# Performance work log

Hardware: AMD Instinct MI355X
Metric: run time of the kernel (lower is better)

Reference implementation:

```python
import jax, jax.numpy as jnp
import numpy as np


def setup_inputs() -> dict:
    key = jax.random.key(0)
    k1, k2 = jax.random.split(key)
    B, L, D = 8, 2048, 256
    x = jax.random.normal(k1, (B, L, D), dtype=jnp.float32)
    x_mask = jax.random.randint(k2, (B, L), 0, 2).astype(bool)  # True = padded key position
    return {"x": x, "x_mask": x_mask}


def reference(x, x_mask):
    # x: [B, L, D], x_mask: [B, L] bool (True = masked/padding)
    B, L, D = x.shape
    # Unscaled self-attention scores: [B, L, L]
    scores = jnp.einsum('bld,bmd->blm', x, x)
    # Diagonal exclusion: score of token with itself set to 0 (not -inf!)
    eye = jnp.eye(L, dtype=bool)
    scores = jnp.where(eye[None, :, :], jnp.float32(0.0), scores)
    # Padding mask: mask key columns with -inf (applied after diagonal zeroing,
    # so a masked diagonal entry ends up -inf, matching the torch order of ops)
    scores = jnp.where(x_mask[:, None, :], -jnp.inf, scores)
    a = jax.nn.softmax(scores, axis=2)
    return jnp.einsum('blm,bmd->bld', a, x)
```

## Files before the change

kernel.cpp:

```cpp
#include <hip/hip_runtime.h>
#include <hip/hip_bf16.h>

#define B_ 8
#define L_ 2048
#define D_ 256
#define BK 32
#define KSPLIT 2
#define KQ (L_/KSPLIT)
#define NIT (KQ/BK)
#define PSTR 40
#define NROW (B_*L_)
#define NE ((size_t)B_*L_*D_)
#define THR 6.0f
#define MINIT (-1e30f)

typedef __attribute__((ext_vector_type(8))) _Float16 f16x8;
typedef __attribute__((ext_vector_type(4))) _Float16 hf4;
typedef __attribute__((ext_vector_type(4))) float f32x4;

#define MFMA16F(a,b,c) __builtin_amdgcn_mfma_f32_16x16x32_f16((a),(b),(c),0,0,0)
#define NEG_INF (-__builtin_inff())
#define GLL(src,dst) __builtin_amdgcn_global_load_lds( \
    (const __attribute__((address_space(1))) void*)(src), \
    (__attribute__((address_space(3))) void*)(dst), 16, 0, 0)

__device__ __forceinline__ f32x4 fmax4(f32x4 a, f32x4 b){
  f32x4 r;
  r[0]=fmaxf(a[0],b[0]); r[1]=fmaxf(a[1],b[1]);
  r[2]=fmaxf(a[2],b[2]); r[3]=fmaxf(a[3],b[3]);
  return r;
}

__global__ void prep_k(const float* __restrict__ x,
                       _Float16* __restrict__ x16,
                       _Float16* __restrict__ vtl){
  __shared__ _Float16 T[64][258];
  const int t = threadIdx.x;
  const int l0 = blockIdx.x*64, b = blockIdx.y;
  const int r = t>>5, c = (t&31)*8;
  #pragma unroll
  for (int p=0;p<8;++p){
    int row = r + p*8;
    size_t idx = ((size_t)(b*L_ + l0 + row))*D_ + c;
    float4 v0 = *(const float4*)(x + idx);
    float4 v1 = *(const float4*)(x + idx + 4);
    f16x8 h;
    h[0]=(_Float16)v0.x; h[1]=(_Float16)v0.y; h[2]=(_Float16)v0.z; h[3]=(_Float16)v0.w;
    h[4]=(_Float16)v1.x; h[5]=(_Float16)v1.y; h[6]=(_Float16)v1.z; h[7]=(_Float16)v1.w;
    *(f16x8*)(x16 + idx) = h;
    #pragma unroll
    for (int j=0;j<8;++j) T[row][c+j] = h[j];
  }
  __syncthreads();
  _Float16* vb = vtl + ((size_t)(b*64 + blockIdx.x*2))*8192;
  #pragma unroll
  for (int i=0;i<8;++i){
    int n = t + 256*i;
    int q = n & 1023, tile = n>>10;
    int d = q>>2, ph = q&3;
    int kc = ph ^ ((d>>1)&3);
    int k0 = tile*32 + kc*8;
    f16x8 h;
    #pragma unroll
    for (int j=0;j<8;++j) h[j] = T[k0+j][d];
    *(f16x8*)(vb + (size_t)n*8) = h;
  }
}

__launch_bounds__(256, 2)
__global__ void flash_k(const _Float16* __restrict__ x16,
                        const _Float16* __restrict__ vtl,
                        const int* __restrict__ mask,
                        _Float16* __restrict__ oall,
                        float* __restrict__ mll,
                        float* __restrict__ mm){
  __shared__ __attribute__((aligned(16))) _Float16 sK[2][8192];
  __shared__ __attribute__((aligned(16))) _Float16 sV[2][8192];
  __shared__ __attribute__((aligned(16))) _Float16 sP[4][16*PSTR];

  const int tid  = threadIdx.x;
  const int wave = tid >> 6, lane = tid & 63;
  const int quad = lane >> 4, l16 = lane & 15;
  const int b = blockIdx.y, z = blockIdx.z;
  const int q0w = blockIdx.x*64 + wave*16;
  const int sw = l16 & 7, vsw = (l16>>1)&3;

  f16x8 qh[8];
  {
    const _Float16* qr = x16 + ((size_t)(b*L_ + q0w + l16))*D_;
    #pragma unroll
    for (int ks=0; ks<8; ++ks)
      qh[ks] = *(const f16x8*)(qr + ks*32 + quad*8);
  }
  unsigned long long mb = 0;
  {
    const int* mrow = mask + b*L_ + z*KQ;
    #pragma unroll
    for (int j=0;j<64;++j)
      mb |= (unsigned long long)(mrow[j*16 + l16] ? 1u : 0u) << j;
  }

  f32x4 M = (f32x4){MINIT, MINIT, MINIT, MINIT};

  unsigned kof[4], vof[4], dof[4];
  #pragma unroll
  for (int i=0;i<4;++i){
    int c = (wave + i*4)*64 + lane;
    int r = c>>5, pk = c&31;
    kof[i] = (unsigned)(r*512 + ((pk ^ (r&7))*16));
    vof[i] = (unsigned)(c*16);
    dof[i] = (unsigned)((wave + i*4)*1024);
  }
  const char* kbase = (const char*)x16 + ((size_t)b*L_ + (size_t)z*KQ)*(D_*2);
  const char* vbase = (const char*)vtl + ((size_t)(b*64 + z*32))*16384;

  #pragma unroll
  for (int i=0;i<4;++i){
    GLL(kbase + kof[i], (char*)sK[0] + dof[i]);
    GLL(vbase + vof[i], (char*)sV[0] + dof[i]);
  }

  f32x4 O[16], Osum;
  #pragma unroll
  for (int i=0;i<16;i++) O[i] = (f32x4){0.f,0.f,0.f,0.f};
  Osum = (f32x4){0.f,0.f,0.f,0.f};
  f16x8 ones;
  #pragma unroll
  for (int j=0;j<8;++j) ones[j] = (_Float16)1.0f;

  __syncthreads();

  for (int it=0; it<NIT; ++it){
    if (it+1 < NIT){
      const char* kb2 = kbase + (size_t)(it+1)*16384;
      const char* vb2 = vbase + (size_t)(it+1)*16384;
      char* kd = (char*)sK[(it+1)&1];
      char* vd = (char*)sV[(it+1)&1];
      #pragma unroll
      for (int i=0;i<4;++i){
        GLL(kb2 + kof[i], kd + dof[i]);
        GLL(vb2 + vof[i], vd + dof[i]);
      }
    }
    const _Float16* kb = sK[it&1];
    const _Float16* vb = sV[it&1];

    f32x4 S[2];
    S[0]=(f32x4){0,0,0,0}; S[1]=(f32x4){0,0,0,0};
    #pragma unroll
    for (int ks=0; ks<8; ++ks){
      f16x8 b0 = *(const f16x8*)(kb + (     l16)*256 + (((ks*4+quad)^sw)*8));
      f16x8 b1 = *(const f16x8*)(kb + (16 + l16)*256 + (((ks*4+quad)^sw)*8));
      S[0] = MFMA16F(qh[ks], b0, S[0]);
      S[1] = MFMA16F(qh[ks], b1, S[1]);
    }

    {
      const int d0 = q0w - (z*KQ + it*BK);
      if ((unsigned)d0 < 32u){
        const int ntd = d0 >> 4;
        #pragma unroll
        for (int r=0;r<4;++r)
          S[ntd][r] = (l16 == quad*4+r) ? 0.0f : S[ntd][r];
      }
    }
    {
      const unsigned mw = (unsigned)(mb >> (unsigned)(it*2));
      const float mk0 = (mw & 1u) ? NEG_INF : 0.0f;
      const float mk1 = (mw & 2u) ? NEG_INF : 0.0f;
      #pragma unroll
      for (int r=0;r<4;++r){ S[0][r] += mk0; S[1][r] += mk1; }
    }

    {
      int ok = 1;
      #pragma unroll
      for (int r=0;r<4;++r){
        ok &= (S[0][r] <= M[r] + THR);
        ok &= (S[1][r] <= M[r] + THR);
      }
      if (!__all(ok)){
        f32x4 t = fmax4(S[0], S[1]);
        #pragma unroll
        for (int off=1; off<16; off<<=1){
          f32x4 o;
          o[0]=__shfl_xor(t[0],off); o[1]=__shfl_xor(t[1],off);
          o[2]=__shfl_xor(t[2],off); o[3]=__shfl_xor(t[3],off);
          t = fmax4(t,o);
        }
        f32x4 mn = fmax4(M, t);
        float sc[4];
        #pragma unroll
        for (int r=0;r<4;++r) sc[r] = __expf(M[r] - mn[r]);
        #pragma unroll
        for (int vt=0; vt<16; ++vt){
          #pragma unroll
          for (int r=0;r<4;++r) O[vt][r] *= sc[r];
        }
        #pragma unroll
        for (int r=0;r<4;++r) Osum[r] *= sc[r];
        M = mn;
      }
    }

    #pragma unroll
    for (int r=0;r<4;++r){
      const int row = quad*4 + r;
      sP[wave][row*PSTR +      l16] = (_Float16)__expf(S[0][r] - M[r]);
      sP[wave][row*PSTR + 16 + l16] = (_Float16)__expf(S[1][r] - M[r]);
    }
    __threadfence_block();
    f16x8 pf = *(const f16x8*)(&sP[wave][l16*PSTR + quad*8]);

    #pragma unroll
    for (int vt=0; vt<16; ++vt){
      f16x8 bv = *(const f16x8*)(vb + (vt*16+l16)*32 + ((quad^vsw)*8));
      O[vt] = MFMA16F(pf, bv, O[vt]);
    }
    Osum = MFMA16F(pf, ones, Osum);

    __syncthreads();
  }

  {
    const int u = b*(L_/16) + blockIdx.x*4 + wave;
    _Float16* ob = oall + (size_t)z*NE + (size_t)u*4096;
    #pragma unroll
    for (int vt=0; vt<16; ++vt){
      hf4 hh;
      #pragma unroll
      for (int r=0;r<4;++r) hh[r] = (_Float16)O[vt][r];
      *(hf4*)(ob + vt*256 + lane*4) = hh;
    }
    if (l16 == 0){
      const int row = u*16 + quad*4;
      #pragma unroll
      for (int r=0;r<4;++r){
        mll[z*NROW + row + r] = Osum[r];
        mm [z*NROW + row + r] = M[r];
      }
    }
  }
}

__global__ void combine_k(float* __restrict__ out,
                          const _Float16* __restrict__ oall,
                          const float* __restrict__ mll,
                          const float* __restrict__ mm){
  __shared__ float T2[16][260];
  const int t = threadIdx.x, u = blockIdx.x;
  const int quad = (t>>4)&3, l16 = t&15;
  const int row0 = u*16 + quad*4;

  f32x4 mz[KSPLIT], lz[KSPLIT];
  #pragma unroll
  for (int zc=0; zc<KSPLIT; ++zc){
    mz[zc] = *(const f32x4*)(mm  + zc*NROW + row0);
    lz[zc] = *(const f32x4*)(mll + zc*NROW + row0);
  }
  f32x4 ms = mz[0];
  #pragma unroll
  for (int zc=1; zc<KSPLIT; ++zc) ms = fmax4(ms, mz[zc]);

  float sc[KSPLIT][4];
  f32x4 den = (f32x4){0.f,0.f,0.f,0.f};
  #pragma unroll
  for (int zc=0; zc<KSPLIT; ++zc){
    #pragma unroll
    for (int r=0;r<4;++r){
      sc[zc][r] = __expf(mz[zc][r] - ms[r]);
      den[r] += sc[zc][r] * lz[zc][r];
    }
  }
  float inv[4];
  #pragma unroll
  for (int r=0;r<4;++r) inv[r] = 1.0f/den[r];

  #pragma unroll
  for (int i=0;i<4;++i){
    const int f = t + 256*i;
    const int vt = f>>6;
    float acc[4] = {0.f,0.f,0.f,0.f};
    #pragma unroll
    for (int zc=0; zc<KSPLIT; ++zc){
      hf4 v = *(const hf4*)(oall + (size_t)zc*NE + (size_t)u*4096 + (size_t)f*4);
      #pragma unroll
      for (int r=0;r<4;++r) acc[r] += sc[zc][r] * (float)v[r];
    }
    #pragma unroll
    for (int r=0;r<4;++r) T2[quad*4+r][vt*16+l16] = acc[r]*inv[r];
  }
  __syncthreads();
  #pragma unroll
  for (int p=0;p<4;++p){
    const int row = (t>>6) + p*4, col = (t&63)*4;
    float4 vv = *(const float4*)&T2[row][col];
    *(float4*)(out + ((size_t)u*16 + row)*D_ + col) = vv;
  }
}

extern "C" void kernel_launch(void* const* d_in, const int* in_sizes, int n_in,
                              void* d_out, int out_size, void* d_ws, size_t ws_size,
                              hipStream_t stream) {
  const float* x    = (const float*)d_in[0];
  const int*   mask = (const int*)d_in[1];
  float*       out  = (float*)d_out;

  _Float16* x16  = (_Float16*)d_ws;
  _Float16* vtl  = x16 + NE;
  _Float16* oall = vtl + NE;
  float*    mll  = (float*)(oall + (size_t)KSPLIT*NE);
  float*    mm   = mll + (size_t)KSPLIT*NROW;

  prep_k   <<<dim3(L_/64, B_), dim3(256), 0, stream>>>(x, x16, vtl);
  flash_k  <<<dim3(L_/64, B_, KSPLIT), dim3(256), 0, stream>>>(x16, vtl, mask, oall, mll, mm);
  combine_k<<<dim3(NROW/16), dim3(256), 0, stream>>>(out, oall, mll, mm);
}
```

Measured before the change: 149.7 us.

## Process 32 query rows per wave to reuse K/V tiles across two query blocks

Each wave now handles two 16-row query blocks (128 queries per workgroup), so every K and V fragment loaded from LDS feeds two MFMAs instead of one. This halves the LDS traffic and global K/V loads per query and halves the grid. In exchange it doubles the O accumulators per wave, drops launch bounds to one block per CU, and leaves 256 workgroups, which lowers occupancy and latency hiding.

```diff
diff --git a/kernel.cpp b/kernel.cpp
--- a/kernel.cpp
+++ b/kernel.cpp
@@ -67,7 +67,7 @@
   }
 }
 
-__launch_bounds__(256, 2)
+__launch_bounds__(256, 1)
 __global__ void flash_k(const _Float16* __restrict__ x16,
                         const _Float16* __restrict__ vtl,
                         const int* __restrict__ mask,
@@ -76,21 +76,23 @@
                         float* __restrict__ mm){
   __shared__ __attribute__((aligned(16))) _Float16 sK[2][8192];
   __shared__ __attribute__((aligned(16))) _Float16 sV[2][8192];
-  __shared__ __attribute__((aligned(16))) _Float16 sP[4][16*PSTR];
+  __shared__ __attribute__((aligned(16))) _Float16 sP[4][32*PSTR];
 
   const int tid  = threadIdx.x;
   const int wave = tid >> 6, lane = tid & 63;
   const int quad = lane >> 4, l16 = lane & 15;
   const int b = blockIdx.y, z = blockIdx.z;
-  const int q0w = blockIdx.x*64 + wave*16;
+  const int q0w = blockIdx.x*128 + wave*32;
   const int sw = l16 & 7, vsw = (l16>>1)&3;
 
-  f16x8 qh[8];
+  f16x8 qh[2][8];
   {
     const _Float16* qr = x16 + ((size_t)(b*L_ + q0w + l16))*D_;
     #pragma unroll
-    for (int ks=0; ks<8; ++ks)
-      qh[ks] = *(const f16x8*)(qr + ks*32 + quad*8);
+    for (int ks=0; ks<8; ++ks){
+      qh[0][ks] = *(const f16x8*)(qr + ks*32 + quad*8);
+      qh[1][ks] = *(const f16x8*)(qr + (size_t)16*D_ + ks*32 + quad*8);
+    }
   }
   unsigned long long mb = 0;
   {
@@ -100,7 +102,9 @@
       mb |= (unsigned long long)(mrow[j*16 + l16] ? 1u : 0u) << j;
   }
 
-  f32x4 M = (f32x4){MINIT, MINIT, MINIT, MINIT};
+  f32x4 M[2];
+  M[0] = (f32x4){MINIT,MINIT,MINIT,MINIT};
+  M[1] = (f32x4){MINIT,MINIT,MINIT,MINIT};
 
   unsigned kof[4], vof[4], dof[4];
   #pragma unroll
@@ -120,10 +124,13 @@
     GLL(vbase + vof[i], (char*)sV[0] + dof[i]);
   }
 
-  f32x4 O[16], Osum;
-  #pragma unroll
-  for (int i=0;i<16;i++) O[i] = (f32x4){0.f,0.f,0.f,0.f};
-  Osum = (f32x4){0.f,0.f,0.f,0.f};
+  f32x4 O[2][16], Osum[2];
+  #pragma unroll
+  for (int qb=0;qb<2;++qb){
+    #pragma unroll
+    for (int i=0;i<16;i++) O[qb][i] = (f32x4){0.f,0.f,0.f,0.f};
+    Osum[qb] = (f32x4){0.f,0.f,0.f,0.f};
+  }
   f16x8 ones;
   #pragma unroll
   for (int j=0;j<8;++j) ones[j] = (_Float16)1.0f;
@@ -145,23 +152,27 @@
     const _Float16* kb = sK[it&1];
     const _Float16* vb = sV[it&1];
 
-    f32x4 S[2];
-    S[0]=(f32x4){0,0,0,0}; S[1]=(f32x4){0,0,0,0};
+    f32x4 S[2][2];
+    S[0][0]=(f32x4){0,0,0,0}; S[0][1]=(f32x4){0,0,0,0};
+    S[1][0]=(f32x4){0,0,0,0}; S[1][1]=(f32x4){0,0,0,0};
     #pragma unroll
     for (int ks=0; ks<8; ++ks){
       f16x8 b0 = *(const f16x8*)(kb + (     l16)*256 + (((ks*4+quad)^sw)*8));
       f16x8 b1 = *(const f16x8*)(kb + (16 + l16)*256 + (((ks*4+quad)^sw)*8));
-      S[0] = MFMA16F(qh[ks], b0, S[0]);
-      S[1] = MFMA16F(qh[ks], b1, S[1]);
+      S[0][0] = MFMA16F(qh[0][ks], b0, S[0][0]);
+      S[1][0] = MFMA16F(qh[1][ks], b0, S[1][0]);
+      S[0][1] = MFMA16F(qh[0][ks], b1, S[0][1]);
+      S[1][1] = MFMA16F(qh[1][ks], b1, S[1][1]);
     }
 
     {
       const int d0 = q0w - (z*KQ + it*BK);
-      if ((unsigned)d0 < 32u){
-        const int ntd = d0 >> 4;
-        #pragma unroll
-        for (int r=0;r<4;++r)
-          S[ntd][r] = (l16 == quad*4+r) ? 0.0f : S[ntd][r];
+      if (d0 == 0){
+        #pragma unroll
+        for (int qb=0;qb<2;++qb)
+          #pragma unroll
+          for (int r=0;r<4;++r)
+            S[qb][qb][r] = (l16 == quad*4+r) ? 0.0f : S[qb][qb][r];
       }
     }
     {
@@ -169,75 +180,88 @@
       const float mk0 = (mw & 1u) ? NEG_INF : 0.0f;
       const float mk1 = (mw & 2u) ? NEG_INF : 0.0f;
       #pragma unroll
-      for (int r=0;r<4;++r){ S[0][r] += mk0; S[1][r] += mk1; }
+      for (int qb=0;qb<2;++qb)
+        #pragma unroll
+        for (int r=0;r<4;++r){ S[qb][0][r] += mk0; S[qb][1][r] += mk1; }
     }
 
     {
+      f32x4 t0 = fmax4(S[0][0], S[0][1]);
+      f32x4 t1 = fmax4(S[1][0], S[1][1]);
       int ok = 1;
       #pragma unroll
       for (int r=0;r<4;++r){
-        ok &= (S[0][r] <= M[r] + THR);
-        ok &= (S[1][r] <= M[r] + THR);
+        ok &= (t0[r] <= M[0][r] + THR);
+        ok &= (t1[r] <= M[1][r] + THR);
       }
       if (!__all(ok)){
-        f32x4 t = fmax4(S[0], S[1]);
         #pragma unroll
         for (int off=1; off<16; off<<=1){
-          f32x4 o;
-          o[0]=__shfl_xor(t[0],off); o[1]=__shfl_xor(t[1],off);
-          o[2]=__shfl_xor(t[2],off); o[3]=__shfl_xor(t[3],off);
-          t = fmax4(t,o);
+          f32x4 o0, o1;
+          #pragma unroll
+          for (int r=0;r<4;++r){ o0[r]=__shfl_xor(t0[r],off); o1[r]=__shfl_xor(t1[r],off); }
+          t0 = fmax4(t0,o0); t1 = fmax4(t1,o1);
         }
-        f32x4 mn = fmax4(M, t);
-        float sc[4];
-        #pragma unroll
-        for (int r=0;r<4;++r) sc[r] = __expf(M[r] - mn[r]);
+        f32x4 mn0 = fmax4(M[0], t0), mn1 = fmax4(M[1], t1);
+        float sc0[4], sc1[4];
+        #pragma unroll
+        for (int r=0;r<4;++r){
+          sc0[r] = __expf(M[0][r] - mn0[r]);
+          sc1[r] = __expf(M[1][r] - mn1[r]);
+        }
         #pragma unroll
         for (int vt=0; vt<16; ++vt){
           #pragma unroll
-          for (int r=0;r<4;++r) O[vt][r] *= sc[r];
+          for (int r=0;r<4;++r){ O[0][vt][r] *= sc0[r]; O[1][vt][r] *= sc1[r]; }
         }
         #pragma unroll
-        for (int r=0;r<4;++r) Osum[r] *= sc[r];
-        M = mn;
-      }
-    }
-
-    #pragma unroll
-    for (int r=0;r<4;++r){
-      const int row = quad*4 + r;
-      sP[wave][row*PSTR +      l16] = (_Float16)__expf(S[0][r] - M[r]);
-      sP[wave][row*PSTR + 16 + l16] = (_Float16)__expf(S[1][r] - M[r]);
+        for (int r=0;r<4;++r){ Osum[0][r] *= sc0[r]; Osum[1][r] *= sc1[r]; }
+        M[0] = mn0; M[1] = mn1;
+      }
+    }
+
+    #pragma unroll
+    for (int qb=0;qb<2;++qb){
+      #pragma unroll
+      for (int r=0;r<4;++r){
+        const int row = qb*16 + quad*4 + r;
+        sP[wave][row*PSTR +      l16] = (_Float16)__expf(S[qb][0][r] - M[qb][r]);
+        sP[wave][row*PSTR + 16 + l16] = (_Float16)__expf(S[qb][1][r] - M[qb][r]);
+      }
     }
     __threadfence_block();
-    f16x8 pf = *(const f16x8*)(&sP[wave][l16*PSTR + quad*8]);
+    f16x8 pf0 = *(const f16x8*)(&sP[wave][(     l16)*PSTR + quad*8]);
+    f16x8 pf1 = *(const f16x8*)(&sP[wave][(16 + l16)*PSTR + quad*8]);
 
     #pragma unroll
     for (int vt=0; vt<16; ++vt){
       f16x8 bv = *(const f16x8*)(vb + (vt*16+l16)*32 + ((quad^vsw)*8));
-      O[vt] = MFMA16F(pf, bv, O[vt]);
-    }
-    Osum = MFMA16F(pf, ones, Osum);
+      O[0][vt] = MFMA16F(pf0, bv, O[0][vt]);
+      O[1][vt] = MFMA16F(pf1, bv, O[1][vt]);
+    }
+    Osum[0] = MFMA16F(pf0, ones, Osum[0]);
+    Osum[1] = MFMA16F(pf1, ones, Osum[1]);
 
     __syncthreads();
   }
 
-  {
-    const int u = b*(L_/16) + blockIdx.x*4 + wave;
+  #pragma unroll
+  for (int qb=0;qb<2;++qb){
+    const int u = b*(L_/16) + blockIdx.x*8 + wave*2 + qb;
     _Float16* ob = oall + (size_t)z*NE + (size_t)u*4096;
     #pragma unroll
     for (int vt=0; vt<16; ++vt){
       hf4 hh;
       #pragma unroll
-      for (int r=0;r<4;++r) hh[r] = (_Float16)O[vt][r];
+      for (int r=0;r<4;++r) hh[r] = (_Float16)O[qb][vt][r];
       *(hf4*)(ob + vt*256 + lane*4) = hh;
     }
     if (l16 == 0){
       const int row = u*16 + quad*4;
       #pragma unroll
       for (int r=0;r<4;++r){
-        mll[z*NROW + row + r] = Osum[r];
-        mm [z*NROW + row + r] = M[r];
+        mll[z*NROW + row + r] = Osum[qb][r];
+        mm [z*NROW + row + r] = M[qb][r];
       }
     }
   }
@@ -313,6 +337,6 @@
   float*    mm   = mll + (size_t)KSPLIT*NROW;
 
   prep_k   <<<dim3(L_/64, B_), dim3(256), 0, stream>>>(x, x16, vtl);
-  flash_k  <<<dim3(L_/64, B_, KSPLIT), dim3(256), 0, stream>>>(x16, vtl, mask, oall, mll, mm);
+  flash_k  <<<dim3(L_/128, B_, KSPLIT), dim3(256), 0, stream>>>(x16, vtl, mask, oall, mll, mm);
   combine_k<<<dim3(NROW/16), dim3(256), 0, stream>>>(out, oall, mll, mm);
 }
```

Measured after the change: 254.7 us. 70.1% more time.

## Software-pipeline the PV MFMA of the previous tile behind the current QK MFMA

Applied to the files above, without the earlier changes.

The P·V product for tile it-1 now runs right after the Q·K^T MFMAs of tile it, so the matrix-core work can overlap the softmax and exponent math instead of waiting behind it. To support this, the P tile in shared memory is double-buffered and the V load is shifted by one iteration, with a final PV step after the loop. The per-block fence is replaced by the existing end-of-iteration barrier. The online-max check is also simplified to test the row maximum once rather than each element. The cost is more live registers and LDS, which may pressure occupancy at the declared launch bounds.

```diff
diff --git a/kernel.cpp b/kernel.cpp
--- a/kernel.cpp
+++ b/kernel.cpp
@@ -76,7 +76,7 @@
                         float* __restrict__ mm){
   __shared__ __attribute__((aligned(16))) _Float16 sK[2][8192];
   __shared__ __attribute__((aligned(16))) _Float16 sV[2][8192];
-  __shared__ __attribute__((aligned(16))) _Float16 sP[4][16*PSTR];
+  __shared__ __attribute__((aligned(16))) _Float16 sP[2][4][16*PSTR];
 
   const int tid  = threadIdx.x;
   const int wave = tid >> 6, lane = tid & 63;
@@ -115,10 +115,7 @@
   const char* vbase = (const char*)vtl + ((size_t)(b*64 + z*32))*16384;
 
   #pragma unroll
-  for (int i=0;i<4;++i){
-    GLL(kbase + kof[i], (char*)sK[0] + dof[i]);
-    GLL(vbase + vof[i], (char*)sV[0] + dof[i]);
-  }
+  for (int i=0;i<4;++i) GLL(kbase + kof[i], (char*)sK[0] + dof[i]);
 
   f32x4 O[16], Osum;
   #pragma unroll
@@ -133,17 +130,17 @@
   for (int it=0; it<NIT; ++it){
     if (it+1 < NIT){
       const char* kb2 = kbase + (size_t)(it+1)*16384;
-      const char* vb2 = vbase + (size_t)(it+1)*16384;
       char* kd = (char*)sK[(it+1)&1];
-      char* vd = (char*)sV[(it+1)&1];
-      #pragma unroll
-      for (int i=0;i<4;++i){
-        GLL(kb2 + kof[i], kd + dof[i]);
-        GLL(vb2 + vof[i], vd + dof[i]);
-      }
+      #pragma unroll
+      for (int i=0;i<4;++i) GLL(kb2 + kof[i], kd + dof[i]);
+    }
+    {
+      const char* vb2 = vbase + (size_t)it*16384;
+      char* vd = (char*)sV[it&1];
+      #pragma unroll
+      for (int i=0;i<4;++i) GLL(vb2 + vof[i], vd + dof[i]);
     }
     const _Float16* kb = sK[it&1];
-    const _Float16* vb = sV[it&1];
 
     f32x4 S[2];
     S[0]=(f32x4){0,0,0,0}; S[1]=(f32x4){0,0,0,0};
@@ -155,6 +152,17 @@
       S[1] = MFMA16F(qh[ks], b1, S[1]);
     }
 
+    if (it > 0){
+      const _Float16* vb = sV[(it-1)&1];
+      f16x8 pf = *(const f16x8*)(&sP[(it-1)&1][wave][l16*PSTR + quad*8]);
+      #pragma unroll
+      for (int vt=0; vt<16; ++vt){
+        f16x8 bv = *(const f16x8*)(vb + (vt*16+l16)*32 + ((quad^vsw)*8));
+        O[vt] = MFMA16F(pf, bv, O[vt]);
+      }
+      Osum = MFMA16F(pf, ones, Osum);
+    }
+
     {
       const int d0 = q0w - (z*KQ + it*BK);
       if ((unsigned)d0 < 32u){
@@ -173,14 +181,11 @@
     }
 
     {
+      f32x4 t = fmax4(S[0], S[1]);
       int ok = 1;
       #pragma unroll
-      for (int r=0;r<4;++r){
-        ok &= (S[0][r] <= M[r] + THR);
-        ok &= (S[1][r] <= M[r] + THR);
-      }
+      for (int r=0;r<4;++r) ok &= (t[r] <= M[r] + THR);
       if (!__all(ok)){
-        f32x4 t = fmax4(S[0], S[1]);
         #pragma unroll
         for (int off=1; off<16; off<<=1){
           f32x4 o;
@@ -206,20 +211,22 @@
     #pragma unroll
     for (int r=0;r<4;++r){
       const int row = quad*4 + r;
-      sP[wave][row*PSTR +      l16] = (_Float16)__expf(S[0][r] - M[r]);
-      sP[wave][row*PSTR + 16 + l16] = (_Float16)__expf(S[1][r] - M[r]);
-    }
-    __threadfence_block();
-    f16x8 pf = *(const f16x8*)(&sP[wave][l16*PSTR + quad*8]);
-
+      sP[it&1][wave][row*PSTR +      l16] = (_Float16)__expf(S[0][r] - M[r]);
+      sP[it&1][wave][row*PSTR + 16 + l16] = (_Float16)__expf(S[1][r] - M[r]);
+    }
+
+    __syncthreads();
+  }
+
+  {
+    const _Float16* vb = sV[(NIT-1)&1];
+    f16x8 pf = *(const f16x8*)(&sP[(NIT-1)&1][wave][l16*PSTR + quad*8]);
     #pragma unroll
     for (int vt=0; vt<16; ++vt){
       f16x8 bv = *(const f16x8*)(vb + (vt*16+l16)*32 + ((quad^vsw)*8));
       O[vt] = MFMA16F(pf, bv, O[vt]);
     }
     Osum = MFMA16F(pf, ones, Osum);
-
-    __syncthreads();
   }
 
   {
```

After: 145.7 us. -2.7%, faster.
